# Kernel tuning notes

Measured on AMD Instinct MI355X. Metric: run time of the kernel, lower is better.

## Reference

```python
import jax, jax.numpy as jnp
import numpy as np

N_NODES = 50000
N_EDGES = 800000
D = 128


def setup_inputs() -> dict:
    key = jax.random.key(0)
    k1, k2, k3, k4 = jax.random.split(key, 4)
    x = jax.random.normal(k1, (N_NODES, D), dtype=jnp.float32)
    src = jax.random.randint(k2, (N_EDGES,), 0, N_NODES, dtype=jnp.int64)
    dst = jax.random.randint(k3, (N_EDGES,), 0, N_NODES, dtype=jnp.int64)
    # nn.Linear(D, D, bias=False): weight shape [out, in]
    W = jax.random.normal(k4, (D, D), dtype=jnp.float32) * (1.0 / np.sqrt(D))
    return {"x": x, "src": src, "dst": dst, "W": W}


def reference(x, src, dst, W):
    h_in = x
    # update_all(copy_src, reduce_sum): gather src features, segment-sum over dst
    agg = jax.ops.segment_sum(x[src], dst, num_segments=N_NODES)  # [N, D]
    h = agg @ W.T                 # Linear(bias=False)
    h = jax.nn.relu(h)            # activation
    h = h + h_in                  # residual (is_normalize=False)
    return h
```

## Files before the change

kernel.cpp:

```cpp
#include <hip/hip_runtime.h>
#include <hip/hip_bf16.h>

#define N_NODES 50000
#define N_EDGES 800000
#define D 128

#define SB     3125
#define SBP    3200
#define WCAP16 384
#define EPB    8192
#define SBLK   98
#define XBLK   800

using bf16x8 = __attribute__((ext_vector_type(8))) short;
using u16x8  = __attribute__((ext_vector_type(8))) unsigned short;
using f32x4  = __attribute__((ext_vector_type(4))) float;

static __device__ __forceinline__ ushort f2bf(float f) {
    __hip_bfloat16 h = __float2bfloat16(f);
    return *reinterpret_cast<ushort*>(&h);
}
static __device__ __forceinline__ float bf2f(ushort u) {
    return __uint_as_float(((unsigned)u) << 16);
}


__global__ void __launch_bounds__(1024)
convert_scatter(const float4* __restrict__ x4, ushort* __restrict__ xb,
                const int* __restrict__ src, const int* __restrict__ dst,
                int* __restrict__ bcnt, unsigned* __restrict__ pairs) {
    __shared__ int      A[SBP];
    __shared__ int      B[SBP];
    __shared__ unsigned payload[EPB];
    const int tid = threadIdx.x;

    if (blockIdx.x >= SBLK) {
        const int gt = (blockIdx.x - SBLK) * 1024 + tid;
        const int total4 = N_NODES * D / 4;
        const int stride = XBLK * 1024;
        for (int j = gt; j < total4; j += stride) {
            float4 v = x4[j];
            ushort4 u = make_ushort4(f2bf(v.x), f2bf(v.y), f2bf(v.z), f2bf(v.w));
            *(ushort4*)(xb + (size_t)j * 4) = u;
        }
        return;
    }

    const int base = blockIdx.x * EPB;
    int nblk = N_EDGES - base;
    if (nblk > EPB) nblk = EPB;

    for (int i = tid; i < SBP; i += 1024) A[i] = 0;
    __syncthreads();

    unsigned pk[8];
#pragma unroll
    for (int k = 0; k < 8; ++k) {
        int i = k * 1024 + tid;
        pk[k] = 0xFFFFFFFFu;
        if (i < nblk) {
            int e = base + i;
            pk[k] = (unsigned)src[e] | ((unsigned)dst[e] << 16);
            atomicAdd(&A[pk[k] >> 20], 1);
        }
    }
    __syncthreads();

    for (int i = tid; i < SBP; i += 1024) B[i] = A[i];
    __syncthreads();

    for (int off = 1; off < SBP; off <<= 1) {
        int t[4];
#pragma unroll
        for (int k = 0; k < 4; ++k) {
            int i = tid + k * 1024;
            t[k] = (i < SBP && i >= off) ? A[i - off] : 0;
        }
        __syncthreads();
#pragma unroll
        for (int k = 0; k < 4; ++k) {
            int i = tid + k * 1024;
            if (i < SBP) A[i] += t[k];
        }
        __syncthreads();
    }

    for (int i = tid; i < SBP; i += 1024) {
        int incl = A[i], cnt = B[i];
        int excl = incl - cnt;
        int gb = cnt ? atomicAdd(&bcnt[i * 16], cnt) : 0;
        A[i] = i * WCAP16 + gb - excl;
        B[i] = excl;
    }
    __syncthreads();

#pragma unroll
    for (int k = 0; k < 8; ++k) {
        unsigned p = pk[k];
        if (p != 0xFFFFFFFFu) {
            int pos = atomicAdd(&B[p >> 20], 1);
            payload[pos] = p;
        }
    }
    __syncthreads();

#pragma unroll
    for (int k = 0; k < 8; ++k) {
        int i = k * 1024 + tid;
        if (i < nblk) {
            unsigned p = payload[i];
            int bkt = (int)(p >> 20);
            int addr = i + A[bkt];
            if (addr < (bkt + 1) * WCAP16)
                pairs[addr] = p;
        }
    }
}

__global__ void __launch_bounds__(256)
gather_sum(const unsigned* __restrict__ pairs, const int* __restrict__ bcnt,
           const ushort* __restrict__ xb, ushort* __restrict__ aggb) {
    __shared__ ushort lsw[4][64];
    const int tid  = threadIdx.x;
    const int wv   = tid >> 6;
    const int lane = tid & 63;
    const int node = blockIdx.x * 4 + wv;
    const int b16  = node >> 4;
    const unsigned sub = (unsigned)(node & 15);

    int cnt = bcnt[b16 * 16];
    if (cnt > WCAP16) cnt = WCAP16;
    const unsigned* wp = pairs + (size_t)b16 * WCAP16;

    int deg = 0;
#pragma unroll
    for (int k = 0; k < 6; ++k) {
        int i = k * 64 + lane;
        unsigned p = (i < cnt) ? wp[i] : 0u;
        bool m = (i < cnt) && (((p >> 16) & 15u) == sub);
        unsigned long long mask = __ballot(m);
        if (m) {
            int rank = deg + __popcll(mask & ((1ULL << lane) - 1ULL));
            if (rank < 64) lsw[wv][rank] = (ushort)(p & 0xFFFFu);
        }
        deg += (int)__popcll(mask);
    }
    if (deg > 64) deg = 64;

    const int q  = lane >> 4;
    const int c8 = (lane & 15) << 3;
    const ushort* xbb = xb + c8;

    float acc[8];
#pragma unroll
    for (int j = 0; j < 8; ++j) acc[j] = 0.f;

    const int full = deg >> 2;
    int t = 0;
    for (; t + 4 <= full; t += 4) {
        int s0 = lsw[wv][4 * t + q];
        int s1 = lsw[wv][4 * t + 4 + q];
        int s2 = lsw[wv][4 * t + 8 + q];
        int s3 = lsw[wv][4 * t + 12 + q];
        u16x8 u0 = *(const u16x8*)(xbb + (size_t)s0 * D);
        u16x8 u1 = *(const u16x8*)(xbb + (size_t)s1 * D);
        u16x8 u2 = *(const u16x8*)(xbb + (size_t)s2 * D);
        u16x8 u3 = *(const u16x8*)(xbb + (size_t)s3 * D);
#pragma unroll
        for (int j = 0; j < 8; ++j)
            acc[j] += (bf2f(u0[j]) + bf2f(u1[j])) + (bf2f(u2[j]) + bf2f(u3[j]));
    }
    for (; t < full; ++t) {
        int s = lsw[wv][4 * t + q];
        u16x8 u = *(const u16x8*)(xbb + (size_t)s * D);
#pragma unroll
        for (int j = 0; j < 8; ++j) acc[j] += bf2f(u[j]);
    }
    const int rem = deg & 3;
    if (rem && q < rem) {
        int s = lsw[wv][4 * full + q];
        u16x8 u = *(const u16x8*)(xbb + (size_t)s * D);
#pragma unroll
        for (int j = 0; j < 8; ++j) acc[j] += bf2f(u[j]);
    }

#pragma unroll
    for (int j = 0; j < 8; ++j) {
        acc[j] += __shfl_xor(acc[j], 16, 64);
        acc[j] += __shfl_xor(acc[j], 32, 64);
    }
    if (q == 0) {
        u16x8 u;
#pragma unroll
        for (int j = 0; j < 8; ++j) u[j] = f2bf(acc[j]);
        *(u16x8*)(aggb + (size_t)node * D + c8) = u;
    }
}

__global__ void __launch_bounds__(256)
gemm_relu_res(const ushort* __restrict__ aggb,
              const float* __restrict__ W,
              const ushort* __restrict__ xb,
              float* __restrict__ out) {
    __shared__ __align__(16) char lds[33792];
    ushort* Wl = (ushort*)lds;

    const int tid  = threadIdx.x;
    const int lane = tid & 63;
    const int wv   = tid >> 6;
    const int m16  = lane & 15;
    const int q    = lane >> 4;

#pragma unroll
    for (int i = 0; i < 8; ++i) {
        int g  = tid + i * 256;
        int o  = g & 127;
        int kc = g >> 7;
        const float4* wp = (const float4*)(W + (size_t)o * D + kc * 8);
        float4 w0 = wp[0], w1 = wp[1];
        bf16x8 hv;
        hv[0] = (short)f2bf(w0.x); hv[1] = (short)f2bf(w0.y);
        hv[2] = (short)f2bf(w0.z); hv[3] = (short)f2bf(w0.w);
        hv[4] = (short)f2bf(w1.x); hv[5] = (short)f2bf(w1.y);
        hv[6] = (short)f2bf(w1.z); hv[7] = (short)f2bf(w1.w);
        *(bf16x8*)&Wl[g * 8] = hv;
    }
    __syncthreads();

    const int nb = blockIdx.x * 64 + wv * 16;
    int arow = nb + m16;
    if (arow >= N_NODES) arow = N_NODES - 1;

    bf16x8 a[4];
#pragma unroll
    for (int kb = 0; kb < 4; ++kb)
        a[kb] = *(const bf16x8*)&aggb[(size_t)arow * D + kb * 32 + q * 8];

    f32x4 acc[8];
#pragma unroll
    for (int t = 0; t < 8; ++t) {
        acc[t] = (f32x4){0.f, 0.f, 0.f, 0.f};
#pragma unroll
        for (int kb = 0; kb < 4; ++kb) {
            bf16x8 bfr = *(const bf16x8*)&Wl[(((kb * 4 + q) * 128) + t * 16 + m16) * 8];
            acc[t] = __builtin_amdgcn_mfma_f32_16x16x32_bf16(a[kb], bfr, acc[t], 0, 0, 0);
        }
    }

    __syncthreads();
    float* Ew = (float*)(lds + wv * 8448);
#pragma unroll
    for (int t = 0; t < 8; ++t)
#pragma unroll
        for (int r = 0; r < 4; ++r)
            Ew[(q * 4 + r) * 132 + t * 16 + m16] = acc[t][r];

    const int h  = lane >> 5;
    const int c4 = (lane & 31) << 2;
#pragma unroll
    for (int j = 0; j < 8; ++j) {
        int r = j * 2 + h;
        int node = nb + r;
        if (node < N_NODES) {
            float4 v  = *(const float4*)&Ew[r * 132 + c4];
            ushort4 xu = *(const ushort4*)(xb + (size_t)node * D + c4);
            float4 o;
            o.x = fmaxf(v.x, 0.f) + bf2f(xu.x);
            o.y = fmaxf(v.y, 0.f) + bf2f(xu.y);
            o.z = fmaxf(v.z, 0.f) + bf2f(xu.z);
            o.w = fmaxf(v.w, 0.f) + bf2f(xu.w);
            *(float4*)(out + (size_t)node * D + c4) = o;
        }
    }
}

__global__ void zero_out(float4* __restrict__ p, int n4) {
    int i = blockIdx.x * 256 + threadIdx.x;
    if (i < n4) p[i] = make_float4(0.f, 0.f, 0.f, 0.f);
}
__global__ void scatter_edges(const float* __restrict__ x,
                              const int* __restrict__ src,
                              const int* __restrict__ dst,
                              float* __restrict__ agg) {
    long long tid = (long long)blockIdx.x * 256 + threadIdx.x;
    if (tid >= (long long)N_EDGES * 32) return;
    int edge = (int)(tid >> 5);
    int c    = ((int)tid & 31) << 2;
    const float4 v = *(const float4*)(x + (size_t)src[edge] * D + c);
    float* p = agg + (size_t)dst[edge] * D + c;
    unsafeAtomicAdd(p + 0, v.x);
    unsafeAtomicAdd(p + 1, v.y);
    unsafeAtomicAdd(p + 2, v.z);
    unsafeAtomicAdd(p + 3, v.w);
}
__global__ void __launch_bounds__(256)
gemm_relu_res_f32(float* data, const float* __restrict__ W,
                  const float* __restrict__ x) {
    __shared__ __align__(16) char lds[50176];
    ushort* Wl = (ushort*)lds;
    ushort* Al = (ushort*)(lds + 32768);
    const int tid  = threadIdx.x;
    const int lane = tid & 63;
    const int wv   = tid >> 6;
    const int m16  = lane & 15;
    const int q    = lane >> 4;
#pragma unroll
    for (int i = 0; i < 8; ++i) {
        int g  = tid + i * 256;
        int o  = g & 127;
        int kc = g >> 7;
        const float4* wp = (const float4*)(W + (size_t)o * D + kc * 8);
        float4 w0 = wp[0], w1 = wp[1];
        bf16x8 hv;
        hv[0] = (short)f2bf(w0.x); hv[1] = (short)f2bf(w0.y);
        hv[2] = (short)f2bf(w0.z); hv[3] = (short)f2bf(w0.w);
        hv[4] = (short)f2bf(w1.x); hv[5] = (short)f2bf(w1.y);
        hv[6] = (short)f2bf(w1.z); hv[7] = (short)f2bf(w1.w);
        *(bf16x8*)&Wl[g * 8] = hv;
    }
    __syncthreads();
    const int nb = blockIdx.x * 64 + wv * 16;
    ushort* Aw = &Al[wv * (16 * 136)];
#pragma unroll
    for (int m = 0; m < 16; ++m) {
        int node = nb + m;
        float2 v = make_float2(0.f, 0.f);
        if (node < N_NODES)
            v = *(const float2*)(data + (size_t)node * D + lane * 2);
        *(ushort2*)&Aw[m * 136 + lane * 2] = make_ushort2(f2bf(v.x), f2bf(v.y));
    }
    bf16x8 a[4];
#pragma unroll
    for (int kb = 0; kb < 4; ++kb)
        a[kb] = *(const bf16x8*)&Aw[m16 * 136 + kb * 32 + q * 8];
    f32x4 acc[8];
#pragma unroll
    for (int t = 0; t < 8; ++t) {
        acc[t] = (f32x4){0.f, 0.f, 0.f, 0.f};
#pragma unroll
        for (int kb = 0; kb < 4; ++kb) {
            bf16x8 bfr = *(const bf16x8*)&Wl[(((kb * 4 + q) * 128) + t * 16 + m16) * 8];
            acc[t] = __builtin_amdgcn_mfma_f32_16x16x32_bf16(a[kb], bfr, acc[t], 0, 0, 0);
        }
    }
    __syncthreads();
    float* Ew = (float*)(lds + wv * 8448);
#pragma unroll
    for (int t = 0; t < 8; ++t)
#pragma unroll
        for (int r = 0; r < 4; ++r)
            Ew[(q * 4 + r) * 132 + t * 16 + m16] = acc[t][r];
    const int h  = lane >> 5;
    const int c4 = (lane & 31) << 2;
#pragma unroll
    for (int j = 0; j < 8; ++j) {
        int r = j * 2 + h;
        int node = nb + r;
        if (node < N_NODES) {
            float4 v  = *(const float4*)&Ew[r * 132 + c4];
            float4 xi = *(const float4*)(x + (size_t)node * D + c4);
            float4 o;
            o.x = fmaxf(v.x, 0.f) + xi.x;
            o.y = fmaxf(v.y, 0.f) + xi.y;
            o.z = fmaxf(v.z, 0.f) + xi.z;
            o.w = fmaxf(v.w, 0.f) + xi.w;
            *(float4*)(data + (size_t)node * D + c4) = o;
        }
    }
}

extern "C" void kernel_launch(void* const* d_in, const int* in_sizes, int n_in,
                              void* d_out, int out_size, void* d_ws, size_t ws_size,
                              hipStream_t stream) {
    const float* x   = (const float*)d_in[0];
    const int*   src = (const int*)d_in[1];
    const int*   dst = (const int*)d_in[2];
    const float* W   = (const float*)d_in[3];
    float* out = (float*)d_out;

    char* ws = (char*)d_ws;
    int*      bcnt  = (int*)ws;      ws += (size_t)SBP * 64;
    unsigned* pairs = (unsigned*)ws; ws += (size_t)SB * WCAP16 * 4;
    ushort*   xb    = (ushort*)ws;   ws += (size_t)N_NODES * D * 2;
    ushort*   aggb  = (ushort*)ws;   ws += (size_t)N_NODES * D * 2;
    const bool big_ws = (ws_size >= (size_t)(ws - (char*)d_ws));

    if (big_ws) {
        hipMemsetAsync(bcnt, 0, (size_t)SBP * 64, stream);
        convert_scatter<<<SBLK + XBLK, 1024, 0, stream>>>(
            (const float4*)x, xb, src, dst, bcnt, pairs);
        gather_sum<<<N_NODES / 4, 256, 0, stream>>>(pairs, bcnt, xb, aggb);
        gemm_relu_res<<<(N_NODES + 63) / 64, 256, 0, stream>>>(aggb, W, xb, out);
    } else {
        int n4 = N_NODES * D / 4;
        zero_out<<<(n4 + 255) / 256, 256, 0, stream>>>((float4*)out, n4);
        long long n_scatter = (long long)N_EDGES * 32;
        scatter_edges<<<(int)((n_scatter + 255) / 256), 256, 0, stream>>>(
            x, src, dst, out);
        gemm_relu_res_f32<<<(N_NODES + 63) / 64, 256, 0, stream>>>(out, W, x);
    }
}
```

Baseline: 154.8 us.

## Split pipeline into per-bucket node sort and column-sharded gather kernels

Separates the x-to-bf16 conversion (which now also zeroes the bucket counters, replacing the memset) from the radix scatter. It adds a node_sort kernel that groups each 16-node bucket's edges by destination into a compact source-index list with offsets and degrees. The gather is then split into four column shards of 32 features, so each block handles 16 nodes on one shard, for better cache locality and parallelism. The GEMM reads the sharded aggregate layout. The cost is two extra launches, extra workspace traffic, and the loss of the overlap between conversion and scatter.

```diff
diff --git a/kernel.cpp b/kernel.cpp
--- a/kernel.cpp
+++ b/kernel.cpp
@@ -10,7 +10,8 @@
 #define WCAP16 384
 #define EPB    8192
 #define SBLK   98
-#define XBLK   800
+#define CONV_BLOCKS 3200
+#define SHARD_STRIDE 1600000
 
 using bf16x8 = __attribute__((ext_vector_type(8))) short;
 using u16x8  = __attribute__((ext_vector_type(8))) unsigned short;
@@ -25,27 +26,27 @@
 }
 
 
+__global__ void __launch_bounds__(256)
+convert_x(const float4* __restrict__ x4, ushort* __restrict__ xb,
+          int* __restrict__ bcnt) {
+    const int gt = blockIdx.x * 256 + threadIdx.x;
+    if (gt < SBP * 16) bcnt[gt] = 0;
+    const int total4 = N_NODES * D / 4;
+    const int stride = CONV_BLOCKS * 256;
+    for (int j = gt; j < total4; j += stride) {
+        float4 v = x4[j];
+        ushort4 u = make_ushort4(f2bf(v.x), f2bf(v.y), f2bf(v.z), f2bf(v.w));
+        *(ushort4*)(xb + (size_t)j * 4) = u;
+    }
+}
+
 __global__ void __launch_bounds__(1024)
-convert_scatter(const float4* __restrict__ x4, ushort* __restrict__ xb,
-                const int* __restrict__ src, const int* __restrict__ dst,
-                int* __restrict__ bcnt, unsigned* __restrict__ pairs) {
+scatter_radix(const int* __restrict__ src, const int* __restrict__ dst,
+              int* __restrict__ bcnt, unsigned* __restrict__ pairs) {
     __shared__ int      A[SBP];
     __shared__ int      B[SBP];
     __shared__ unsigned payload[EPB];
     const int tid = threadIdx.x;
-
-    if (blockIdx.x >= SBLK) {
-        const int gt = (blockIdx.x - SBLK) * 1024 + tid;
-        const int total4 = N_NODES * D / 4;
-        const int stride = XBLK * 1024;
-        for (int j = gt; j < total4; j += stride) {
-            float4 v = x4[j];
-            ushort4 u = make_ushort4(f2bf(v.x), f2bf(v.y), f2bf(v.z), f2bf(v.w));
-            *(ushort4*)(xb + (size_t)j * 4) = u;
-        }
-        return;
-    }
-
     const int base = blockIdx.x * EPB;
     int nblk = N_EDGES - base;
     if (nblk > EPB) nblk = EPB;
@@ -118,87 +119,96 @@
 }
 
 __global__ void __launch_bounds__(256)
-gather_sum(const unsigned* __restrict__ pairs, const int* __restrict__ bcnt,
-           const ushort* __restrict__ xb, ushort* __restrict__ aggb) {
-    __shared__ ushort lsw[4][64];
-    const int tid  = threadIdx.x;
-    const int wv   = tid >> 6;
-    const int lane = tid & 63;
-    const int node = blockIdx.x * 4 + wv;
-    const int b16  = node >> 4;
-    const unsigned sub = (unsigned)(node & 15);
-
-    int cnt = bcnt[b16 * 16];
+node_sort(const unsigned* __restrict__ pairs, const int* __restrict__ bcnt,
+          ushort* __restrict__ snode, int* __restrict__ od) {
+    __shared__ ushort buf[WCAP16];
+    __shared__ int h16[16], cur16[16];
+    const int b = blockIdx.x, tid = threadIdx.x;
+    int cnt = bcnt[b * 16];
     if (cnt > WCAP16) cnt = WCAP16;
-    const unsigned* wp = pairs + (size_t)b16 * WCAP16;
-
-    int deg = 0;
-#pragma unroll
-    for (int k = 0; k < 6; ++k) {
-        int i = k * 64 + lane;
-        unsigned p = (i < cnt) ? wp[i] : 0u;
-        bool m = (i < cnt) && (((p >> 16) & 15u) == sub);
-        unsigned long long mask = __ballot(m);
-        if (m) {
-            int rank = deg + __popcll(mask & ((1ULL << lane) - 1ULL));
-            if (rank < 64) lsw[wv][rank] = (ushort)(p & 0xFFFFu);
-        }
-        deg += (int)__popcll(mask);
-    }
-    if (deg > 64) deg = 64;
-
-    const int q  = lane >> 4;
-    const int c8 = (lane & 15) << 3;
-    const ushort* xbb = xb + c8;
-
-    float acc[8];
-#pragma unroll
-    for (int j = 0; j < 8; ++j) acc[j] = 0.f;
-
-    const int full = deg >> 2;
-    int t = 0;
-    for (; t + 4 <= full; t += 4) {
-        int s0 = lsw[wv][4 * t + q];
-        int s1 = lsw[wv][4 * t + 4 + q];
-        int s2 = lsw[wv][4 * t + 8 + q];
-        int s3 = lsw[wv][4 * t + 12 + q];
-        u16x8 u0 = *(const u16x8*)(xbb + (size_t)s0 * D);
-        u16x8 u1 = *(const u16x8*)(xbb + (size_t)s1 * D);
-        u16x8 u2 = *(const u16x8*)(xbb + (size_t)s2 * D);
-        u16x8 u3 = *(const u16x8*)(xbb + (size_t)s3 * D);
-#pragma unroll
-        for (int j = 0; j < 8; ++j)
-            acc[j] += (bf2f(u0[j]) + bf2f(u1[j])) + (bf2f(u2[j]) + bf2f(u3[j]));
-    }
-    for (; t < full; ++t) {
-        int s = lsw[wv][4 * t + q];
-        u16x8 u = *(const u16x8*)(xbb + (size_t)s * D);
-#pragma unroll
-        for (int j = 0; j < 8; ++j) acc[j] += bf2f(u[j]);
-    }
-    const int rem = deg & 3;
-    if (rem && q < rem) {
-        int s = lsw[wv][4 * full + q];
-        u16x8 u = *(const u16x8*)(xbb + (size_t)s * D);
-#pragma unroll
-        for (int j = 0; j < 8; ++j) acc[j] += bf2f(u[j]);
-    }
-
-#pragma unroll
-    for (int j = 0; j < 8; ++j) {
-        acc[j] += __shfl_xor(acc[j], 16, 64);
-        acc[j] += __shfl_xor(acc[j], 32, 64);
-    }
-    if (q == 0) {
-        u16x8 u;
-#pragma unroll
-        for (int j = 0; j < 8; ++j) u[j] = f2bf(acc[j]);
-        *(u16x8*)(aggb + (size_t)node * D + c8) = u;
-    }
+    unsigned p0 = 0xFFFFFFFFu, p1 = 0xFFFFFFFFu;
+    if (tid < cnt)       p0 = pairs[b * WCAP16 + tid];
+    if (tid + 256 < cnt) p1 = pairs[b * WCAP16 + 256 + tid];
+    if (tid < 16) h16[tid] = 0;
+    __syncthreads();
+    if (p0 != 0xFFFFFFFFu) atomicAdd(&h16[(p0 >> 16) & 15], 1);
+    if (p1 != 0xFFFFFFFFu) atomicAdd(&h16[(p1 >> 16) & 15], 1);
+    __syncthreads();
+    if (tid < 16) {
+        int v = h16[tid], incl = v;
+#pragma unroll
+        for (int o = 1; o < 16; o <<= 1) {
+            int t = __shfl_up(incl, o, 64);
+            if (tid >= o) incl += t;
+        }
+        int excl = incl - v;
+        cur16[tid] = excl;
+        od[b * 16 + tid] = excl | (v << 16);
+    }
+    __syncthreads();
+    if (p0 != 0xFFFFFFFFu) { int pos = atomicAdd(&cur16[(p0 >> 16) & 15], 1); buf[pos] = (ushort)(p0 & 0xFFFFu); }
+    if (p1 != 0xFFFFFFFFu) { int pos = atomicAdd(&cur16[(p1 >> 16) & 15], 1); buf[pos] = (ushort)(p1 & 0xFFFFu); }
+    __syncthreads();
+    if (tid < cnt)       snode[b * WCAP16 + tid]       = buf[tid];
+    if (tid + 256 < cnt) snode[b * WCAP16 + 256 + tid] = buf[tid + 256];
 }
 
 __global__ void __launch_bounds__(256)
-gemm_relu_res(const ushort* __restrict__ aggb,
+gather_shard(const ushort* __restrict__ snode, const int* __restrict__ od,
+             const ushort* __restrict__ xb, ushort* __restrict__ aggS) {
+    __shared__ ushort lsw[WCAP16];
+    __shared__ int od16[16];
+    const int tid = threadIdx.x;
+    const int b = blockIdx.x >> 2;
+    const int s = blockIdx.x & 3;
+    if (tid < WCAP16 / 4)
+        ((ushort4*)lsw)[tid] = ((const ushort4*)(snode + (size_t)b * WCAP16))[tid];
+    if (tid < 16) od16[tid] = od[b * 16 + tid];
+    __syncthreads();
+
+    const int wv = tid >> 6, lane = tid & 63;
+    const int es = lane >> 2, sub = lane & 3;
+    const ushort* xs = xb + s * 32 + sub * 8;
+
+#pragma unroll 1
+    for (int k = wv * 4; k < wv * 4 + 4; ++k) {
+        const int o = od16[k];
+        const int beg = o & 0xFFFF, deg = o >> 16;
+        float acc[8];
+#pragma unroll
+        for (int j = 0; j < 8; ++j) acc[j] = 0.f;
+
+        const int steps = (deg + 15) >> 4;
+#pragma unroll 1
+        for (int t = 0; t < steps; ++t) {
+            int slot = t * 16 + es;
+            int idx = beg + ((slot < deg) ? slot : 0);
+            int sn = lsw[idx];
+            u16x8 u = *(const u16x8*)(xs + (size_t)sn * D);
+            if (slot < deg) {
+#pragma unroll
+                for (int j = 0; j < 8; ++j) acc[j] += bf2f(u[j]);
+            }
+        }
+#pragma unroll
+        for (int j = 0; j < 8; ++j) {
+            acc[j] += __shfl_xor(acc[j], 4, 64);
+            acc[j] += __shfl_xor(acc[j], 8, 64);
+            acc[j] += __shfl_xor(acc[j], 16, 64);
+            acc[j] += __shfl_xor(acc[j], 32, 64);
+        }
+        if (lane < 4) {
+            u16x8 u;
+#pragma unroll
+            for (int j = 0; j < 8; ++j) u[j] = f2bf(acc[j]);
+            *(u16x8*)(aggS + (size_t)s * SHARD_STRIDE
+                      + (size_t)(b * 16 + k) * 32 + lane * 8) = u;
+        }
+    }
+}
+
+__global__ void __launch_bounds__(256)
+gemm_relu_res(const ushort* __restrict__ aggS,
               const float* __restrict__ W,
               const ushort* __restrict__ xb,
               float* __restrict__ out) {
@@ -234,7 +244,8 @@
     bf16x8 a[4];
 #pragma unroll
     for (int kb = 0; kb < 4; ++kb)
-        a[kb] = *(const bf16x8*)&aggb[(size_t)arow * D + kb * 32 + q * 8];
+        a[kb] = *(const bf16x8*)&aggS[(size_t)kb * SHARD_STRIDE
+                                      + (size_t)arow * 32 + q * 8];
 
     f32x4 acc[8];
 #pragma unroll
@@ -381,16 +392,18 @@
     char* ws = (char*)d_ws;
     int*      bcnt  = (int*)ws;      ws += (size_t)SBP * 64;
     unsigned* pairs = (unsigned*)ws; ws += (size_t)SB * WCAP16 * 4;
+    ushort*   snode = (ushort*)ws;   ws += (size_t)SB * WCAP16 * 2;
+    int*      od    = (int*)ws;      ws += (size_t)SB * 16 * 4;
     ushort*   xb    = (ushort*)ws;   ws += (size_t)N_NODES * D * 2;
-    ushort*   aggb  = (ushort*)ws;   ws += (size_t)N_NODES * D * 2;
+    ushort*   aggS  = (ushort*)ws;   ws += (size_t)4 * SHARD_STRIDE * 2;
     const bool big_ws = (ws_size >= (size_t)(ws - (char*)d_ws));
 
     if (big_ws) {
-        hipMemsetAsync(bcnt, 0, (size_t)SBP * 64, stream);
-        convert_scatter<<<SBLK + XBLK, 1024, 0, stream>>>(
-            (const float4*)x, xb, src, dst, bcnt, pairs);
-        gather_sum<<<N_NODES / 4, 256, 0, stream>>>(pairs, bcnt, xb, aggb);
-        gemm_relu_res<<<(N_NODES + 63) / 64, 256, 0, stream>>>(aggb, W, xb, out);
+        convert_x<<<CONV_BLOCKS, 256, 0, stream>>>((const float4*)x, xb, bcnt);
+        scatter_radix<<<SBLK, 1024, 0, stream>>>(src, dst, bcnt, pairs);
+        node_sort<<<SB, 256, 0, stream>>>(pairs, bcnt, snode, od);
+        gather_shard<<<SB * 4, 256, 0, stream>>>(snode, od, xb, aggS);
+        gemm_relu_res<<<(N_NODES + 63) / 64, 256, 0, stream>>>(aggS, W, xb, out);
     } else {
         int n4 = N_NODES * D / 4;
         zero_out<<<(n4 + 255) / 256, 256, 0, stream>>>((float4*)out, n4);
```

Measured after the change: 200.6 us. 1.3x slower.
